# Kernel tuning notes

Hardware: AMD Instinct MI355X
Metric: run time of the kernel (lower is better)

## Reference

```python
import jax, jax.numpy as jnp
import numpy as np

B, T, H, V = 4, 1024, 2048, 32000
BETA, EPS_LO, EPS_HI, TEMP = 0.1, 0.2, 0.2, 1.0


def setup_inputs() -> dict:
    key = jax.random.key(0)
    ks = jax.random.split(key, 7)
    x = jax.random.normal(ks[0], (B, T, H), jnp.float32)
    ref_input = jax.random.normal(ks[1], (B, T, H), jnp.float32)
    lin_weight = jax.random.normal(ks[2], (V, H), jnp.float32) * 0.02
    ref_lin_weight = jax.random.normal(ks[3], (V, H), jnp.float32) * 0.02
    selected_token_ids = jax.random.randint(ks[4], (B, T), 0, V, dtype=jnp.int32)
    attention_mask = jnp.ones((B, T), jnp.int32)
    advantages = jax.random.normal(ks[5], (B,), jnp.float32)
    # plausible stale log-probs near -log(V) so importance ratio ~ 1
    old_per_token_logps = jax.random.normal(ks[6], (B, T), jnp.float32) * 0.05 - float(np.log(V))
    return dict(x=x, ref_input=ref_input, lin_weight=lin_weight,
                ref_lin_weight=ref_lin_weight, selected_token_ids=selected_token_ids,
                attention_mask=attention_mask, advantages=advantages,
                old_per_token_logps=old_per_token_logps)


def _per_token_logps(h, W, ids):
    # fused linear + log-softmax, gathered at the sampled token ids
    logits = jnp.einsum('bth,vh->btv', h, W) / TEMP          # (B,T,V)
    lse = jax.nn.logsumexp(logits, axis=-1)                   # (B,T)
    sel = jnp.take_along_axis(logits, ids[..., None], axis=-1)[..., 0]
    return sel - lse


def reference(x, ref_input, lin_weight, ref_lin_weight, selected_token_ids,
              attention_mask, advantages, old_per_token_logps):
    per_token_logps = _per_token_logps(x, lin_weight, selected_token_ids)
    # reference model runs without grad in the original (torch.no_grad)
    ref_logps = jax.lax.stop_gradient(
        _per_token_logps(ref_input, ref_lin_weight, selected_token_ids))

    coef1 = jnp.exp(per_token_logps - old_per_token_logps)   # importance ratio
    coef2 = jnp.clip(coef1, 1.0 - EPS_LO, 1.0 + EPS_HI)
    adv = advantages[:, None]                                 # (B,1)
    per_token_loss = -jnp.minimum(coef1 * adv, coef2 * adv)

    delta = ref_logps - per_token_logps
    kl = jnp.exp(delta) - delta - 1.0                         # k3 KL estimator
    per_token_loss = per_token_loss + BETA * kl

    m = attention_mask.astype(per_token_loss.dtype)
    loss = jnp.sum(per_token_loss * m) / jnp.maximum(jnp.sum(m), 1.0)
    return loss
```

## Files before the change

kernel.cpp:

```cpp
#include <hip/hip_runtime.h>
#include <hip/hip_bf16.h>
#include <stdint.h>

#define B_    4
#define T_    1024
#define H_    2048
#define V_    32000
#define M_TOK (B_ * T_)
#define BM    256
#define BN    256
#define BK    64
#define NVT   (V_ / BN)
#define KT    (H_ / BK)
#define KT2   (KT / 2)
#define TILE_E (BM * BK)
#define BETA_   0.1f
#define EPS_LO_ 0.2f
#define EPS_HI_ 0.2f

typedef __bf16 bf16x8 __attribute__((ext_vector_type(8)));
typedef float  f32x4  __attribute__((ext_vector_type(4)));

__device__ __forceinline__ void load16_lds(const void* g, void* l) {
    __builtin_amdgcn_global_load_lds(
        (const __attribute__((address_space(1))) unsigned int*)g,
        (__attribute__((address_space(3))) unsigned int*)l, 16, 0, 0);
}

__device__ __forceinline__ unsigned short f2bf(float f) {
    unsigned u = __float_as_uint(f);
    u += 0x7FFF + ((u >> 16) & 1);
    return (unsigned short)(u >> 16);
}
__device__ __forceinline__ unsigned pack2(float a, float b) {
    return (unsigned)f2bf(a) | ((unsigned)f2bf(b) << 16);
}

__global__ __launch_bounds__(256) void cvt_bf16(const float4* __restrict__ in,
                                                uint4* __restrict__ out, int n8) {
    int i = blockIdx.x * blockDim.x + threadIdx.x;
    if (i >= n8) return;
    float4 a = in[2 * i];
    float4 b = in[2 * i + 1];
    uint4 r;
    r.x = pack2(a.x, a.y);
    r.y = pack2(a.z, a.w);
    r.z = pack2(b.x, b.y);
    r.w = pack2(b.z, b.w);
    out[i] = r;
}

__global__ __launch_bounds__(512, 2) void gemm_lse(
    const unsigned short* __restrict__ Xp, const unsigned short* __restrict__ Wp,
    const unsigned short* __restrict__ Xr, const unsigned short* __restrict__ Wr,
    const int* __restrict__ ids,
    float* __restrict__ part_p, float* __restrict__ part_r,
    float* __restrict__ sel_p,  float* __restrict__ sel_r)
{
    const int tid  = threadIdx.x;
    const int lane = tid & 63;
    const int wid  = tid >> 6;
    const int wm   = wid >> 2;
    const int wn   = wid & 3;
    const int tm   = blockIdx.x;
    const int tn   = blockIdx.y;
    const int z    = blockIdx.z;

    const unsigned short* X = z ? Xr : Xp;
    const unsigned short* W = z ? Wr : Wp;
    float* part = z ? part_r : part_p;
    float* sel  = z ? sel_r  : sel_p;

    const int rowA = tm * BM;
    const int colB = tn * BN;

    __shared__ __align__(16) unsigned short As[2 * TILE_E];
    __shared__ __align__(16) unsigned short Bs[2 * TILE_E];

    const int g0 = wid * 2;
    const int lr = lane >> 3;
    const int ls = lane & 7;
    const int so = (ls ^ lr) * 8;
    const int a0 = (g0 >> 3) * 128 + (g0 & 7) * 8;
    const int b0 = (g0 >> 2) * 64  + (g0 & 3) * 8;
    const unsigned short* pA[2];
    const unsigned short* pB[2];
    pA[0] = X + (size_t)(rowA + a0 + lr) * H_ + so;
    pA[1] = pA[0] + (size_t)64 * H_;
    pB[0] = W + (size_t)(colB + b0 + lr) * H_ + so;
    pB[1] = pB[0] + (size_t)32 * H_;
    const int aL[2] = { a0 * BK, a0 * BK + 64 * BK };
    const int bL[2] = { b0 * BK, b0 * BK + 32 * BK };

    const int lo = lane & 15;
    const int hi = lane >> 4;
    const int offs0 = ((hi) ^ (lane & 7)) * 8;
    const int offs1 = offs0 ^ 32;

    bf16x8 aR[4][2];
    bf16x8 bR[2][2][2];
    f32x4  acc[8][4] = {};

#define FENCE() asm volatile("" ::: "memory")
#define BARRIER() do { FENCE(); __builtin_amdgcn_s_barrier(); FENCE(); } while (0)

#define STAGE_A(H, BUF, KOFF) do { \
    load16_lds(pA[H] + (KOFF),          &As[(BUF)*TILE_E + aL[H]]); \
    load16_lds(pA[H] + 8*H_ + (KOFF),   &As[(BUF)*TILE_E + aL[H] + 8*BK]); \
} while (0)
#define STAGE_B(H, BUF, KOFF) do { \
    load16_lds(pB[H] + (KOFF),          &Bs[(BUF)*TILE_E + bL[H]]); \
    load16_lds(pB[H] + 8*H_ + (KOFF),   &Bs[(BUF)*TILE_E + bL[H] + 8*BK]); \
} while (0)

#define RD_A(QM, BUF) do { \
    _Pragma("unroll") \
    for (int fmi = 0; fmi < 4; ++fmi) { \
        const unsigned short* p_ = &As[(BUF)*TILE_E + (wm*128 + ((QM)*4 + fmi)*16 + lo)*BK]; \
        aR[fmi][0] = *(const bf16x8*)(p_ + offs0); \
        aR[fmi][1] = *(const bf16x8*)(p_ + offs1); \
    } \
} while (0)
#define RD_B(QN, BUF) do { \
    _Pragma("unroll") \
    for (int fni = 0; fni < 2; ++fni) { \
        const unsigned short* p_ = &Bs[(BUF)*TILE_E + (wn*64 + ((QN)*2 + fni)*16 + lo)*BK]; \
        bR[QN][fni][0] = *(const bf16x8*)(p_ + offs0); \
        bR[QN][fni][1] = *(const bf16x8*)(p_ + offs1); \
    } \
} while (0)

#define MFMA16(QM, QN) do { \
    _Pragma("unroll") \
    for (int fmi = 0; fmi < 4; ++fmi) { \
        _Pragma("unroll") \
        for (int fni = 0; fni < 2; ++fni) { \
            f32x4 c_ = acc[(QM)*4 + fmi][(QN)*2 + fni]; \
            c_ = __builtin_amdgcn_mfma_f32_16x16x32_bf16(aR[fmi][0], bR[QN][fni][0], c_, 0, 0, 0); \
            c_ = __builtin_amdgcn_mfma_f32_16x16x32_bf16(aR[fmi][1], bR[QN][fni][1], c_, 0, 0, 0); \
            acc[(QM)*4 + fmi][(QN)*2 + fni] = c_; \
        } \
    } \
} while (0)

#define MFMA_PHASE(QM, QN) do { \
    BARRIER(); \
    __builtin_amdgcn_s_setprio(1); \
    MFMA16(QM, QN); \
    __builtin_amdgcn_s_setprio(0); \
} while (0)

    STAGE_A(0, 0, 0);
    STAGE_B(0, 0, 0);
    STAGE_B(1, 0, 0);
    STAGE_A(1, 0, 0);
    STAGE_A(0, 1, BK);
    STAGE_B(0, 1, BK);
    STAGE_B(1, 1, BK);
    asm volatile("s_waitcnt vmcnt(6)" ::: "memory");
    BARRIER();

    for (int i = 0; i < KT2; ++i) {
        const int k1 = (2 * i + 1) * BK;
        const int k2 = (2 * i + 2 < KT ? 2 * i + 2 : KT - 1) * BK;
        const int k3 = (2 * i + 3 < KT ? 2 * i + 3 : KT - 1) * BK;
        RD_A(0, 0); RD_B(0, 0);
        STAGE_A(1, 1, k1);
        MFMA_PHASE(0, 0);
        BARRIER();
        RD_B(1, 0);
        STAGE_A(0, 0, k2);
        MFMA_PHASE(0, 1);
        BARRIER();
        RD_A(1, 0);
        STAGE_B(0, 0, k2);
        MFMA_PHASE(1, 0);
        BARRIER();
        STAGE_B(1, 0, k2);
        MFMA_PHASE(1, 1);
        asm volatile("s_waitcnt vmcnt(6)" ::: "memory");
        BARRIER();
        RD_A(0, 1); RD_B(0, 1);
        STAGE_A(1, 0, k2);
        MFMA_PHASE(0, 0);
        BARRIER();
        RD_B(1, 1);
        STAGE_A(0, 1, k3);
        MFMA_PHASE(0, 1);
        BARRIER();
        RD_A(1, 1);
        STAGE_B(0, 1, k3);
        MFMA_PHASE(1, 0);
        BARRIER();
        STAGE_B(1, 1, k3);
        MFMA_PHASE(1, 1);
        asm volatile("s_waitcnt vmcnt(6)" ::: "memory");
        BARRIER();
    }

#undef FENCE
#undef BARRIER
#undef STAGE_A
#undef STAGE_B
#undef RD_A
#undef RD_B
#undef MFMA16
#undef MFMA_PHASE

    __syncthreads();
    float* sums_f = (float*)As;
    int*   ids_e  = (int*)Bs;
    if (tid < BM) ids_e[tid] = ids[rowA + tid];
    __syncthreads();

    #pragma unroll
    for (int fm = 0; fm < 8; ++fm) {
        float r4[4];
        #pragma unroll
        for (int reg = 0; reg < 4; ++reg) {
            const int row_l = wm * 128 + fm * 16 + hi * 4 + reg;
            const int id    = ids_e[row_l];
            float s = 0.f;
            #pragma unroll
            for (int fn = 0; fn < 4; ++fn) {
                float v = acc[fm][fn][reg];
                int col_g = colB + wn * 64 + fn * 16 + lo;
                if (id == col_g) sel[rowA + row_l] = v;
                s += __expf(v);
            }
            r4[reg] = s;
        }
        #pragma unroll
        for (int m = 1; m < 16; m <<= 1) {
            #pragma unroll
            for (int reg = 0; reg < 4; ++reg)
                r4[reg] += __shfl_xor(r4[reg], m, 64);
        }
        if (lo == 0) {
            #pragma unroll
            for (int reg = 0; reg < 4; ++reg)
                sums_f[wn * BM + wm * 128 + fm * 16 + hi * 4 + reg] = r4[reg];
        }
    }
    __syncthreads();
    if (tid < BM) {
        float tot = sums_f[tid] + sums_f[BM + tid] + sums_f[2 * BM + tid] + sums_f[3 * BM + tid];
        part[(size_t)(rowA + tid) * NVT + tn] = tot;
    }
}

__global__ __launch_bounds__(256) void finalize(
    const float* __restrict__ pp, const float* __restrict__ pr,
    const float* __restrict__ sp, const float* __restrict__ sr,
    const int* __restrict__ mask, const float* __restrict__ adv,
    const float* __restrict__ oldlp,
    float* __restrict__ bsum, float* __restrict__ bmsum)
{
    const int lane = threadIdx.x & 63;
    const int wid  = threadIdx.x >> 6;
    const int t    = blockIdx.x * 4 + wid;

    float s_p = 0.f, s_r = 0.f;
    for (int i = lane; i < NVT; i += 64) {
        s_p += pp[(size_t)t * NVT + i];
        s_r += pr[(size_t)t * NVT + i];
    }
    #pragma unroll
    for (int k = 1; k < 64; k <<= 1) {
        s_p += __shfl_xor(s_p, k, 64);
        s_r += __shfl_xor(s_r, k, 64);
    }
    __shared__ float ls[4], ms[4];
    if (lane == 0) {
        float p  = sp[t] - logf(s_p);
        float r  = sr[t] - logf(s_r);
        float c1 = expf(p - oldlp[t]);
        float c2 = fminf(fmaxf(c1, 1.0f - EPS_LO_), 1.0f + EPS_HI_);
        float a  = adv[t >> 10];
        float ptl = -fminf(c1 * a, c2 * a);
        float d   = r - p;
        ptl += BETA_ * (expf(d) - d - 1.0f);
        float mm = (float)mask[t];
        ls[wid] = ptl * mm;
        ms[wid] = mm;
    }
    __syncthreads();
    if (threadIdx.x == 0) {
        bsum[blockIdx.x]  = ls[0] + ls[1] + ls[2] + ls[3];
        bmsum[blockIdx.x] = ms[0] + ms[1] + ms[2] + ms[3];
    }
}

__global__ __launch_bounds__(256) void final_reduce(
    const float* __restrict__ bs, const float* __restrict__ bm, float* __restrict__ out)
{
    const int tid = threadIdx.x;
    float s = 0.f, m = 0.f;
    for (int i = tid; i < M_TOK / 4; i += 256) { s += bs[i]; m += bm[i]; }
    #pragma unroll
    for (int k = 1; k < 64; k <<= 1) {
        s += __shfl_xor(s, k, 64);
        m += __shfl_xor(m, k, 64);
    }
    __shared__ float ss[4], sm[4];
    if ((tid & 63) == 0) { ss[tid >> 6] = s; sm[tid >> 6] = m; }
    __syncthreads();
    if (tid == 0) {
        float S = ss[0] + ss[1] + ss[2] + ss[3];
        float M = sm[0] + sm[1] + sm[2] + sm[3];
        out[0] = S / fmaxf(M, 1.0f);
    }
}

extern "C" void kernel_launch(void* const* d_in, const int* in_sizes, int n_in,
                              void* d_out, int out_size, void* d_ws, size_t ws_size,
                              hipStream_t stream) {
    const float* x     = (const float*)d_in[0];
    const float* rx    = (const float*)d_in[1];
    const float* w     = (const float*)d_in[2];
    const float* rw    = (const float*)d_in[3];
    const int*   ids   = (const int*)d_in[4];
    const int*   mask  = (const int*)d_in[5];
    const float* adv   = (const float*)d_in[6];
    const float* oldlp = (const float*)d_in[7];
    float* out = (float*)d_out;

    char* ws = (char*)d_ws;
    size_t off = 0;
    auto alloc = [&](size_t bytes) -> void* {
        void* p = ws + off;
        off += (bytes + 255) & ~(size_t)255;
        return p;
    };
    unsigned short* xb   = (unsigned short*)alloc((size_t)M_TOK * H_ * 2);
    unsigned short* rxb  = (unsigned short*)alloc((size_t)M_TOK * H_ * 2);
    unsigned short* wb   = (unsigned short*)alloc((size_t)V_ * H_ * 2);
    unsigned short* rwb  = (unsigned short*)alloc((size_t)V_ * H_ * 2);
    float* pp    = (float*)alloc((size_t)M_TOK * NVT * 4);
    float* pr    = (float*)alloc((size_t)M_TOK * NVT * 4);
    float* sp    = (float*)alloc((size_t)M_TOK * 4);
    float* sr    = (float*)alloc((size_t)M_TOK * 4);
    float* bsum  = (float*)alloc((M_TOK / 4) * 4);
    float* bmsum = (float*)alloc((M_TOK / 4) * 4);

    const int n8x = M_TOK * H_ / 8;
    const int n8w = V_ * H_ / 8;
    cvt_bf16<<<(n8x + 255) / 256, 256, 0, stream>>>((const float4*)x,  (uint4*)xb,  n8x);
    cvt_bf16<<<(n8x + 255) / 256, 256, 0, stream>>>((const float4*)rx, (uint4*)rxb, n8x);
    cvt_bf16<<<(n8w + 255) / 256, 256, 0, stream>>>((const float4*)w,  (uint4*)wb,  n8w);
    cvt_bf16<<<(n8w + 255) / 256, 256, 0, stream>>>((const float4*)rw, (uint4*)rwb, n8w);

    dim3 grid(M_TOK / BM, NVT, 2);
    gemm_lse<<<grid, 512, 0, stream>>>(xb, wb, rxb, rwb, ids, pp, pr, sp, sr);

    finalize<<<M_TOK / 4, 256, 0, stream>>>(pp, pr, sp, sr, mask, adv, oldlp, bsum, bmsum);
    final_reduce<<<1, 256, 0, stream>>>(bsum, bmsum, out);
}
```

Measured before the change: 1.800 ms.

## Fuse bf16 conversions, remap GEMM tiles per XCD, reuse B fragments across phases

```diff
diff --git a/kernel.cpp b/kernel.cpp
--- a/kernel.cpp
+++ b/kernel.cpp
@@ -36,18 +36,31 @@
     return (unsigned)f2bf(a) | ((unsigned)f2bf(b) << 16);
 }
 
-__global__ __launch_bounds__(256) void cvt_bf16(const float4* __restrict__ in,
-                                                uint4* __restrict__ out, int n8) {
-    int i = blockIdx.x * blockDim.x + threadIdx.x;
-    if (i >= n8) return;
-    float4 a = in[2 * i];
-    float4 b = in[2 * i + 1];
-    uint4 r;
-    r.x = pack2(a.x, a.y);
-    r.y = pack2(a.z, a.w);
-    r.z = pack2(b.x, b.y);
-    r.w = pack2(b.z, b.w);
-    out[i] = r;
+#define N8X 1048576
+#define N8W 8192000
+__global__ __launch_bounds__(256) void cvt_all(
+    const float4* __restrict__ x,  const float4* __restrict__ rx,
+    const float4* __restrict__ w,  const float4* __restrict__ rw,
+    uint4* __restrict__ xb, uint4* __restrict__ rxb,
+    uint4* __restrict__ wb, uint4* __restrict__ rwb)
+{
+    const int total = 2 * N8X + 2 * N8W;
+    for (int i = blockIdx.x * blockDim.x + threadIdx.x; i < total;
+         i += gridDim.x * blockDim.x) {
+        const float4* src; uint4* dst; int j;
+        if (i < N8X)                { src = x;  dst = xb;  j = i; }
+        else if (i < 2 * N8X)       { src = rx; dst = rxb; j = i - N8X; }
+        else if (i < 2 * N8X + N8W) { src = w;  dst = wb;  j = i - 2 * N8X; }
+        else                        { src = rw; dst = rwb; j = i - 2 * N8X - N8W; }
+        float4 a = src[2 * j];
+        float4 b = src[2 * j + 1];
+        uint4 r;
+        r.x = pack2(a.x, a.y);
+        r.y = pack2(a.z, a.w);
+        r.z = pack2(b.x, b.y);
+        r.w = pack2(b.z, b.w);
+        dst[j] = r;
+    }
 }
 
 __global__ __launch_bounds__(512, 2) void gemm_lse(
@@ -62,9 +75,14 @@
     const int wid  = tid >> 6;
     const int wm   = wid >> 2;
     const int wn   = wid & 3;
-    const int tm   = blockIdx.x;
-    const int tn   = blockIdx.y;
-    const int z    = blockIdx.z;
+
+    const int lid = blockIdx.x + (int)gridDim.x * (blockIdx.y + (int)gridDim.y * blockIdx.z);
+    const int xcd = lid & 7;
+    const int seq = lid >> 3;
+    const int z   = seq / 250;
+    const int pos = seq % 250;
+    const int tm  = xcd * 2 + pos / 125;
+    const int tn  = pos % 125;
 
     const unsigned short* X = z ? Xr : Xp;
     const unsigned short* W = z ? Wr : Wp;
@@ -94,59 +112,57 @@
 
     const int lo = lane & 15;
     const int hi = lane >> 4;
-    const int offs0 = ((hi) ^ (lane & 7)) * 8;
+    const int offs0 = (hi ^ (lane & 7)) * 8;
     const int offs1 = offs0 ^ 32;
 
-    bf16x8 aR[4][2];
-    bf16x8 bR[2][2][2];
+    bf16x8 aF[4][2];
+    bf16x8 b0f[2][2];
+    bf16x8 b1f[2][2];
     f32x4  acc[8][4] = {};
 
-#define FENCE() asm volatile("" ::: "memory")
-#define BARRIER() do { FENCE(); __builtin_amdgcn_s_barrier(); FENCE(); } while (0)
+#define BAR() do { asm volatile("" ::: "memory"); \
+                   __builtin_amdgcn_s_barrier(); \
+                   asm volatile("" ::: "memory"); } while (0)
+#define VMCNT6() asm volatile("s_waitcnt vmcnt(6)" ::: "memory")
 
 #define STAGE_A(H, BUF, KOFF) do { \
-    load16_lds(pA[H] + (KOFF),          &As[(BUF)*TILE_E + aL[H]]); \
-    load16_lds(pA[H] + 8*H_ + (KOFF),   &As[(BUF)*TILE_E + aL[H] + 8*BK]); \
+    load16_lds(pA[H] + (KOFF),        &As[(BUF)*TILE_E + aL[H]]); \
+    load16_lds(pA[H] + 8*H_ + (KOFF), &As[(BUF)*TILE_E + aL[H] + 8*BK]); \
 } while (0)
 #define STAGE_B(H, BUF, KOFF) do { \
-    load16_lds(pB[H] + (KOFF),          &Bs[(BUF)*TILE_E + bL[H]]); \
-    load16_lds(pB[H] + 8*H_ + (KOFF),   &Bs[(BUF)*TILE_E + bL[H] + 8*BK]); \
-} while (0)
-
-#define RD_A(QM, BUF) do { \
+    load16_lds(pB[H] + (KOFF),        &Bs[(BUF)*TILE_E + bL[H]]); \
+    load16_lds(pB[H] + 8*H_ + (KOFF), &Bs[(BUF)*TILE_E + bL[H] + 8*BK]); \
+} while (0)
+
+#define RD_AF(QM, BUF) do { \
     _Pragma("unroll") \
     for (int fmi = 0; fmi < 4; ++fmi) { \
         const unsigned short* p_ = &As[(BUF)*TILE_E + (wm*128 + ((QM)*4 + fmi)*16 + lo)*BK]; \
-        aR[fmi][0] = *(const bf16x8*)(p_ + offs0); \
-        aR[fmi][1] = *(const bf16x8*)(p_ + offs1); \
+        aF[fmi][0] = *(const bf16x8*)(p_ + offs0); \
+        aF[fmi][1] = *(const bf16x8*)(p_ + offs1); \
     } \
 } while (0)
-#define RD_B(QN, BUF) do { \
+#define RD_BQ(DST, QN, BUF) do { \
     _Pragma("unroll") \
     for (int fni = 0; fni < 2; ++fni) { \
         const unsigned short* p_ = &Bs[(BUF)*TILE_E + (wn*64 + ((QN)*2 + fni)*16 + lo)*BK]; \
-        bR[QN][fni][0] = *(const bf16x8*)(p_ + offs0); \
-        bR[QN][fni][1] = *(const bf16x8*)(p_ + offs1); \
+        DST[fni][0] = *(const bf16x8*)(p_ + offs0); \
+        DST[fni][1] = *(const bf16x8*)(p_ + offs1); \
     } \
 } while (0)
 
-#define MFMA16(QM, QN) do { \
+#define MM(QM, BQ, CB) do { \
+    __builtin_amdgcn_s_setprio(1); \
     _Pragma("unroll") \
     for (int fmi = 0; fmi < 4; ++fmi) { \
         _Pragma("unroll") \
         for (int fni = 0; fni < 2; ++fni) { \
-            f32x4 c_ = acc[(QM)*4 + fmi][(QN)*2 + fni]; \
-            c_ = __builtin_amdgcn_mfma_f32_16x16x32_bf16(aR[fmi][0], bR[QN][fni][0], c_, 0, 0, 0); \
-            c_ = __builtin_amdgcn_mfma_f32_16x16x32_bf16(aR[fmi][1], bR[QN][fni][1], c_, 0, 0, 0); \
-            acc[(QM)*4 + fmi][(QN)*2 + fni] = c_; \
+            f32x4 c_ = acc[(QM)*4 + fmi][(CB) + fni]; \
+            c_ = __builtin_amdgcn_mfma_f32_16x16x32_bf16(aF[fmi][0], BQ[fni][0], c_, 0, 0, 0); \
+            c_ = __builtin_amdgcn_mfma_f32_16x16x32_bf16(aF[fmi][1], BQ[fni][1], c_, 0, 0, 0); \
+            acc[(QM)*4 + fmi][(CB) + fni] = c_; \
         } \
     } \
-} while (0)
-
-#define MFMA_PHASE(QM, QN) do { \
-    BARRIER(); \
-    __builtin_amdgcn_s_setprio(1); \
-    MFMA16(QM, QN); \
     __builtin_amdgcn_s_setprio(0); \
 } while (0)
 
@@ -157,55 +173,53 @@
     STAGE_A(0, 1, BK);
     STAGE_B(0, 1, BK);
     STAGE_B(1, 1, BK);
-    asm volatile("s_waitcnt vmcnt(6)" ::: "memory");
-    BARRIER();
+    VMCNT6();
 
     for (int i = 0; i < KT2; ++i) {
         const int k1 = (2 * i + 1) * BK;
         const int k2 = (2 * i + 2 < KT ? 2 * i + 2 : KT - 1) * BK;
         const int k3 = (2 * i + 3 < KT ? 2 * i + 3 : KT - 1) * BK;
-        RD_A(0, 0); RD_B(0, 0);
+        BAR();
+        RD_AF(0, 0); RD_BQ(b0f, 0, 0);
         STAGE_A(1, 1, k1);
-        MFMA_PHASE(0, 0);
-        BARRIER();
-        RD_B(1, 0);
+        MM(0, b0f, 0);
+        BAR();
+        RD_BQ(b1f, 1, 0);
         STAGE_A(0, 0, k2);
-        MFMA_PHASE(0, 1);
-        BARRIER();
-        RD_A(1, 0);
+        MM(0, b1f, 2);
+        BAR();
+        RD_AF(1, 0);
         STAGE_B(0, 0, k2);
-        MFMA_PHASE(1, 0);
-        BARRIER();
+        MM(1, b0f, 0);
+        BAR();
         STAGE_B(1, 0, k2);
-        MFMA_PHASE(1, 1);
-        asm volatile("s_waitcnt vmcnt(6)" ::: "memory");
-        BARRIER();
-        RD_A(0, 1); RD_B(0, 1);
+        MM(1, b1f, 2);
+        VMCNT6();
+        BAR();
+        RD_AF(0, 1); RD_BQ(b0f, 0, 1);
         STAGE_A(1, 0, k2);
-        MFMA_PHASE(0, 0);
-        BARRIER();
-        RD_B(1, 1);
+        MM(0, b0f, 0);
+        BAR();
+        RD_BQ(b1f, 1, 1);
         STAGE_A(0, 1, k3);
-        MFMA_PHASE(0, 1);
-        BARRIER();
-        RD_A(1, 1);
+        MM(0, b1f, 2);
+        BAR();
+        RD_AF(1, 1);
         STAGE_B(0, 1, k3);
-        MFMA_PHASE(1, 0);
-        BARRIER();
+        MM(1, b0f, 0);
+        BAR();
         STAGE_B(1, 1, k3);
-        MFMA_PHASE(1, 1);
-        asm volatile("s_waitcnt vmcnt(6)" ::: "memory");
-        BARRIER();
-    }
-
-#undef FENCE
-#undef BARRIER
+        MM(1, b1f, 2);
+        VMCNT6();
+    }
+
+#undef BAR
+#undef VMCNT6
 #undef STAGE_A
 #undef STAGE_B
-#undef RD_A
-#undef RD_B
-#undef MFMA16
-#undef MFMA_PHASE
+#undef RD_AF
+#undef RD_BQ
+#undef MM
 
     __syncthreads();
     float* sums_f = (float*)As;
@@ -343,12 +357,9 @@
     float* bsum  = (float*)alloc((M_TOK / 4) * 4);
     float* bmsum = (float*)alloc((M_TOK / 4) * 4);
 
-    const int n8x = M_TOK * H_ / 8;
-    const int n8w = V_ * H_ / 8;
-    cvt_bf16<<<(n8x + 255) / 256, 256, 0, stream>>>((const float4*)x,  (uint4*)xb,  n8x);
-    cvt_bf16<<<(n8x + 255) / 256, 256, 0, stream>>>((const float4*)rx, (uint4*)rxb, n8x);
-    cvt_bf16<<<(n8w + 255) / 256, 256, 0, stream>>>((const float4*)w,  (uint4*)wb,  n8w);
-    cvt_bf16<<<(n8w + 255) / 256, 256, 0, stream>>>((const float4*)rw, (uint4*)rwb, n8w);
+    cvt_all<<<2048, 256, 0, stream>>>((const float4*)x, (const float4*)rx,
+                                      (const float4*)w, (const float4*)rw,
+                                      (uint4*)xb, (uint4*)rxb, (uint4*)wb, (uint4*)rwb);
 
     dim3 grid(M_TOK / BM, NVT, 2);
     gemm_lse<<<grid, 512, 0, stream>>>(xb, wb, rxb, rwb, ids, pp, pr, sp, sr);
```

Measured after the change: 1.685 ms. -6.4%, faster.
